# Optimization experiments

Hardware: AMD Instinct MI355X
Metric: run time of the kernel (lower is better)

## Reference

```python
import jax, jax.numpy as jnp
import numpy as np

N_NODES = 100000
N_EDGES = 3200000
N_GRAPHS = 512


def setup_inputs() -> dict:
    key = jax.random.key(0)
    ks = jax.random.split(key, 10)
    x = jax.random.normal(ks[0], (N_NODES, 2), dtype=jnp.float32)
    edge_index = jax.random.randint(ks[1], (2, N_EDGES), 0, N_NODES, dtype=jnp.int32)
    batch = jnp.sort(jax.random.randint(ks[2], (N_NODES,), 0, N_GRAPHS, dtype=jnp.int32))

    def glorot(k, shape):
        fan_in, fan_out = shape
        s = jnp.sqrt(6.0 / (fan_in + fan_out)).astype(jnp.float32)
        return jax.random.uniform(k, shape, jnp.float32, -s, s)

    return {
        "x": x,
        "edge_index": edge_index,
        "batch": batch,
        "W1": glorot(ks[3], (2, 16)),  "b1": jnp.zeros((16,), jnp.float32),
        "W2": glorot(ks[4], (16, 32)), "b2": jnp.zeros((32,), jnp.float32),
        "W3": glorot(ks[5], (32, 48)), "b3": jnp.zeros((48,), jnp.float32),
        "Wl1": glorot(ks[6], (48, 24)), "bl1": jnp.zeros((24,), jnp.float32),
        "Wl2": glorot(ks[7], (24, 10)), "bl2": jnp.zeros((10,), jnp.float32),
    }


def reference(x, edge_index, batch, W1, b1, W2, b2, W3, b3, Wl1, bl1, Wl2, bl2):
    n = x.shape[0]
    loop = jnp.arange(n, dtype=edge_index.dtype)
    # GCNConv adds self-loops, then symmetric normalization D^{-1/2} A_hat D^{-1/2}
    src = jnp.concatenate([edge_index[0], loop])  # [E+N]
    dst = jnp.concatenate([edge_index[1], loop])  # [E+N]
    deg = jax.ops.segment_sum(jnp.ones(src.shape[0], x.dtype), dst, num_segments=n)
    dis = jax.lax.rsqrt(deg)  # deg >= 1 thanks to self-loops
    norm = (dis[src] * dis[dst])[:, None]  # [E+N, 1]

    def gcn(h, W, b):
        h = h @ W  # transform first (small channel dims)
        msg = norm * h[src]  # gather + edge scale
        return jax.ops.segment_sum(msg, dst, num_segments=n) + b  # scatter-add

    h = jax.nn.relu(gcn(x, W1, b1))   # [N, 16]
    h = jax.nn.relu(gcn(h, W2, b2))   # [N, 32]
    h = jax.nn.relu(gcn(h, W3, b3))   # [N, 48]
    pooled = jax.ops.segment_max(h, batch, num_segments=N_GRAPHS)  # [G, 48]
    pooled = jnp.where(jnp.isfinite(pooled), pooled, 0.0)  # empty segments -> 0
    h = jax.nn.relu(pooled @ Wl1 + bl1)  # [G, 24]
    return h @ Wl2 + bl2  # [G, 10]
```

## Files before the change

kernel.cpp:

```cpp
#include <hip/hip_runtime.h>
#include <hip/hip_bf16.h>


#define THREADS 256
#define NBSHIFT 7
#define NPB 128
#define MAXNB 1024
#define SCAT_T 8192
#define SCAT_K 32


__global__ void bkt_count(const int* __restrict__ dst, int* __restrict__ bktCnt,
                          int nE, int nb) {
    __shared__ int h[MAXNB];
    for (int i = threadIdx.x; i < nb; i += blockDim.x) h[i] = 0;
    __syncthreads();
    for (long e = blockIdx.x * blockDim.x + threadIdx.x; e < nE;
         e += (long)gridDim.x * blockDim.x)
        atomicAdd(&h[dst[e] >> NBSHIFT], 1);
    __syncthreads();
    for (int i = threadIdx.x; i < nb; i += blockDim.x)
        if (h[i]) atomicAdd(&bktCnt[i], h[i]);
}

__global__ void bkt_scan(const int* __restrict__ bktCnt, int* __restrict__ bktBase,
                         int* __restrict__ bktCursor, int nb) {
    __shared__ int sm[MAXNB];
    int t = threadIdx.x;
    int v = (t < nb) ? bktCnt[t] : 0;
    sm[t] = v;
    __syncthreads();
    for (int o = 1; o < MAXNB; o <<= 1) {
        int add = (t >= o) ? sm[t - o] : 0;
        __syncthreads();
        sm[t] += add;
        __syncthreads();
    }
    if (t < nb) {
        int b = sm[t] - v;
        bktBase[t] = b;
        bktCursor[t] = b;
    }
}

__global__ void bkt_scatter(const int* __restrict__ src, const int* __restrict__ dst,
                            int* __restrict__ bktCursor, unsigned* __restrict__ barr,
                            int nE, int nb) {
    __shared__ int h[MAXNB];
    __shared__ int base[MAXNB];
    long t0 = (long)blockIdx.x * SCAT_T;
    for (int i = threadIdx.x; i < nb; i += blockDim.x) h[i] = 0;
    __syncthreads();
    unsigned pk[SCAT_K];
    int br[SCAT_K];
#pragma unroll
    for (int k = 0; k < SCAT_K; ++k) {
        long e = t0 + (long)k * 256 + threadIdx.x;
        if (e < nE) {
            int d = dst[e], s = src[e];
            int b = d >> NBSHIFT;
            int r = atomicAdd(&h[b], 1);
            pk[k] = (unsigned)s | ((unsigned)(d & (NPB - 1)) << 20);
            br[k] = (b << 13) | r;
        } else {
            br[k] = -1;
        }
    }
    __syncthreads();
    for (int i = threadIdx.x; i < nb; i += blockDim.x) {
        int c = h[i];
        base[i] = c ? atomicAdd(&bktCursor[i], c) : 0;
    }
    __syncthreads();
#pragma unroll
    for (int k = 0; k < SCAT_K; ++k) {
        if (br[k] >= 0) {
            int b = br[k] >> 13, r = br[k] & 8191;
            barr[(long)base[b] + r] = pk[k];
        }
    }
}

__global__ void bkt_sort(const int* __restrict__ bktBase, const int* __restrict__ bktCnt,
                         const unsigned* __restrict__ barr, int* __restrict__ col,
                         int* __restrict__ deg, int* __restrict__ rowstart, int n) {
    __shared__ int h[NPB], inc[NPB], c2[NPB];
    int b = blockIdx.x;
    int node0 = b << NBSHIFT;
    int nlocal = min(NPB, n - node0);
    int t = threadIdx.x;
    if (t < NPB) { h[t] = 0; c2[t] = 0; }
    __syncthreads();
    int base = bktBase[b], cnt = bktCnt[b];
    for (int i = t; i < cnt; i += blockDim.x)
        atomicAdd(&h[(barr[(long)base + i] >> 20) & (NPB - 1)], 1);
    __syncthreads();
    if (t < NPB) inc[t] = h[t];
    __syncthreads();
    for (int o = 1; o < NPB; o <<= 1) {
        int add = (t >= o && t < NPB) ? inc[t - o] : 0;
        __syncthreads();
        if (t < NPB) inc[t] += add;
        __syncthreads();
    }
    if (t < nlocal) {
        int node = node0 + t;
        deg[node] = h[t];
        rowstart[node] = base + inc[t] - h[t];
    }
    __syncthreads();
    for (int i = t; i < cnt; i += blockDim.x) {
        unsigned w = barr[(long)base + i];
        int dl = (w >> 20) & (NPB - 1);
        int r = atomicAdd(&c2[dl], 1);
        col[(long)base + inc[dl] - h[dl] + r] = (int)(w & 0xFFFFF);
    }
}

__global__ void dis_kernel(const int* __restrict__ deg, float* __restrict__ dis, int n) {
    int i = blockIdx.x * blockDim.x + threadIdx.x;
    if (i < n) dis[i] = 1.0f / sqrtf((float)(deg[i] + 1));
}


__global__ void pre1_kernel(const float* __restrict__ x, const float* __restrict__ dis,
                            float* __restrict__ g, int n) {
    int i = blockIdx.x * blockDim.x + threadIdx.x;
    if (i >= n) return;
    float d = dis[i];
    float2 v = ((const float2*)x)[i];
    v.x *= d; v.y *= d;
    ((float2*)g)[i] = v;
}

template <int CIN, int COUT>
__global__ void pre_kernel(const float* __restrict__ accPrev, const float* __restrict__ dis,
                           const float* __restrict__ W, const float* __restrict__ b,
                           float* __restrict__ g, int n) {
    int i = blockIdx.x * blockDim.x + threadIdx.x;
    if (i >= n) return;
    float d = dis[i];
    float a[CIN];
#pragma unroll
    for (int k = 0; k < CIN; ++k) a[k] = d * accPrev[(long)i * CIN + k];
    float o[COUT];
#pragma unroll
    for (int c = 0; c < COUT; ++c) o[c] = b[c];
#pragma unroll
    for (int k = 0; k < CIN; ++k) {
        float ak = a[k];
#pragma unroll
        for (int c = 0; c < COUT; ++c) o[c] += ak * W[k * COUT + c];
    }
#pragma unroll
    for (int c = 0; c < COUT; ++c) g[(long)i * COUT + c] = d * fmaxf(o[c], 0.0f);
}

template <int CIN, int COUT>
__global__ void final_kernel(const float* __restrict__ accPrev, const float* __restrict__ dis,
                             const float* __restrict__ W, const float* __restrict__ b,
                             float* __restrict__ h, int n) {
    int i = blockIdx.x * blockDim.x + threadIdx.x;
    if (i >= n) return;
    float d = dis[i];
    float a[CIN];
#pragma unroll
    for (int k = 0; k < CIN; ++k) a[k] = d * accPrev[(long)i * CIN + k];
    float o[COUT];
#pragma unroll
    for (int c = 0; c < COUT; ++c) o[c] = b[c];
#pragma unroll
    for (int k = 0; k < CIN; ++k) {
        float ak = a[k];
#pragma unroll
        for (int c = 0; c < COUT; ++c) o[c] += ak * W[k * COUT + c];
    }
#pragma unroll
    for (int c = 0; c < COUT; ++c) h[(long)i * COUT + c] = fmaxf(o[c], 0.0f);
}

template <int CIN>
__global__ void gather_kernel(const int* __restrict__ rowstart, const int* __restrict__ deg,
                              const int* __restrict__ col, const float* __restrict__ g,
                              float* __restrict__ acc, int n) {
    int gtid = blockIdx.x * blockDim.x + threadIdx.x;
    int node = gtid >> 6;
    int lane = threadIdx.x & 63;
    if (node >= n) return;
    constexpr int EPW = 64 / CIN;
    int c = lane % CIN;
    int es = lane / CIN;
    int base = rowstart[node];
    int dg = deg[node];
    float sum = 0.0f;
    for (int j = es; j < dg; j += EPW) {
        int s = col[base + j];
        sum += g[(long)s * CIN + c];
    }
#pragma unroll
    for (int m = CIN; m < 64; m <<= 1) sum += __shfl_xor(sum, m);
    if (lane < CIN) acc[(long)node * CIN + c] = g[(long)node * CIN + c] + sum;
}

template <int CIN>
__global__ void gather4_kernel(const int* __restrict__ rowstart, const int* __restrict__ deg,
                               const int* __restrict__ col, const float* __restrict__ g,
                               float* __restrict__ acc, int n) {
    constexpr int LPE = CIN / 4;
    constexpr int EPW = 64 / LPE;
    int gtid = blockIdx.x * blockDim.x + threadIdx.x;
    int node = gtid >> 6;
    int lane = threadIdx.x & 63;
    if (node >= n) return;
    int c4 = lane & (LPE - 1);
    int es = lane / LPE;
    int base = rowstart[node];
    int dg = deg[node];
    float4 sum = make_float4(0.f, 0.f, 0.f, 0.f);
    for (int j = es; j < dg; j += EPW) {
        int s = col[base + j];
        float4 v = ((const float4*)g)[(long)s * LPE + c4];
        sum.x += v.x; sum.y += v.y; sum.z += v.z; sum.w += v.w;
    }
#pragma unroll
    for (int m = LPE; m < 64; m <<= 1) {
        sum.x += __shfl_xor(sum.x, m);
        sum.y += __shfl_xor(sum.y, m);
        sum.z += __shfl_xor(sum.z, m);
        sum.w += __shfl_xor(sum.w, m);
    }
    if (lane < LPE) {
        float4 self = ((const float4*)g)[(long)node * LPE + c4];
        float4 r = make_float4(self.x + sum.x, self.y + sum.y,
                               self.z + sum.z, self.w + sum.w);
        ((float4*)acc)[(long)node * LPE + c4] = r;
    }
}

__global__ void pool_kernel(const float* __restrict__ h, const int* __restrict__ batch,
                            unsigned* __restrict__ pooled, int n) {
    const int C = 48, K = 16;
    int tid = blockIdx.x * blockDim.x + threadIdx.x;
    int chunk = tid / C, c = tid % C;
    int j0 = chunk * K;
    if (j0 >= n) return;
    int jend = min(j0 + K, n);
    int cur = batch[j0];
    float m = 0.0f;
    for (int j = j0; j < jend; ++j) {
        int gph = batch[j];
        if (gph != cur) {
            atomicMax(&pooled[cur * C + c], __float_as_uint(m));
            cur = gph;
            m = 0.0f;
        }
        m = fmaxf(m, h[(long)j * C + c]);
    }
    atomicMax(&pooled[cur * C + c], __float_as_uint(m));
}

__global__ void mlp_kernel(const unsigned* __restrict__ pooled, const float* __restrict__ Wl1,
                           const float* __restrict__ bl1, const float* __restrict__ Wl2,
                           const float* __restrict__ bl2, float* __restrict__ out, int G) {
    __shared__ float sW1[48 * 24];
    __shared__ float sW2[24 * 10];
    __shared__ float sp[4][48];
    __shared__ float sh[4][24];
    int t = threadIdx.x;
    int sub = t >> 6;
    int lane = t & 63;
    int g = blockIdx.x * 4 + sub;
    for (int i = t; i < 48 * 24; i += 256) sW1[i] = Wl1[i];
    for (int i = t; i < 24 * 10; i += 256) sW2[i] = Wl2[i];
    if (g < G && lane < 48) sp[sub][lane] = __uint_as_float(pooled[g * 48 + lane]);
    __syncthreads();
    if (g < G && lane < 24) {
        float a = bl1[lane];
#pragma unroll
        for (int k = 0; k < 48; ++k) a += sp[sub][k] * sW1[k * 24 + lane];
        sh[sub][lane] = fmaxf(a, 0.0f);
    }
    __syncthreads();
    if (g < G && lane < 10) {
        float a = bl2[lane];
#pragma unroll
        for (int j = 0; j < 24; ++j) a += sh[sub][j] * sW2[j * 10 + lane];
        out[g * 10 + lane] = a;
    }
}

static inline int cdiv(long a, int b) { return (int)((a + b - 1) / b); }

extern "C" void kernel_launch(void* const* d_in, const int* in_sizes, int n_in,
                              void* d_out, int out_size, void* d_ws, size_t ws_size,
                              hipStream_t stream) {
    const float* x = (const float*)d_in[0];
    const int* ei = (const int*)d_in[1];
    const int* batch = (const int*)d_in[2];
    const float* W1 = (const float*)d_in[3];
    const float* b1 = (const float*)d_in[4];
    const float* W2 = (const float*)d_in[5];
    const float* b2 = (const float*)d_in[6];
    const float* W3 = (const float*)d_in[7];
    const float* b3 = (const float*)d_in[8];
    const float* Wl1 = (const float*)d_in[9];
    const float* bl1 = (const float*)d_in[10];
    const float* Wl2 = (const float*)d_in[11];
    const float* bl2 = (const float*)d_in[12];
    float* out = (float*)d_out;

    const int N = in_sizes[0] / 2;
    const int E = in_sizes[1] / 2;
    const int G = out_size / 10;
    const int nb = cdiv(N, NPB);

    const int* src = ei;
    const int* dst = ei + E;

    char* w = (char*)d_ws;
    size_t off = 0;
    auto alloc = [&](size_t bytes) {
        void* p = w + off;
        off = (off + bytes + 255) & ~(size_t)255;
        return p;
    };
    int* bktCnt = (int*)alloc((size_t)MAXNB * 4);
    int* bktBase = (int*)alloc((size_t)MAXNB * 4);
    int* bktCursor = (int*)alloc((size_t)MAXNB * 4);
    size_t shared_bytes = ((size_t)E * 4 > (size_t)N * 48 * 4) ? (size_t)E * 4
                                                               : (size_t)N * 48 * 4;
    void* shared_region = alloc(shared_bytes);
    unsigned* barr = (unsigned*)shared_region;
    float* h3 = (float*)shared_region;
    int* col = (int*)alloc((size_t)E * 4);
    int* deg = (int*)alloc((size_t)N * 4);
    float* dis = (float*)alloc((size_t)N * 4);
    int* rowstart = (int*)alloc((size_t)N * 4);
    float* g = (float*)alloc((size_t)N * 32 * 4);
    float* acc = (float*)alloc((size_t)N * 32 * 4);
    unsigned* pooled = (unsigned*)alloc((size_t)G * 48 * 4);
    (void)ws_size;

    hipMemsetAsync(bktCnt, 0, (size_t)MAXNB * 4, stream);
    hipMemsetAsync(pooled, 0, (size_t)G * 48 * 4, stream);

    bkt_count<<<512, THREADS, 0, stream>>>(dst, bktCnt, E, nb);
    bkt_scan<<<1, MAXNB, 0, stream>>>(bktCnt, bktBase, bktCursor, nb);
    bkt_scatter<<<cdiv(E, SCAT_T), THREADS, 0, stream>>>(src, dst, bktCursor, barr, E, nb);
    bkt_sort<<<nb, THREADS, 0, stream>>>(bktBase, bktCnt, barr, col, deg, rowstart, N);
    dis_kernel<<<cdiv(N, THREADS), THREADS, 0, stream>>>(deg, dis, N);

    pre1_kernel<<<cdiv(N, THREADS), THREADS, 0, stream>>>(x, dis, g, N);
    gather_kernel<2><<<cdiv((long)N * 64, THREADS), THREADS, 0, stream>>>(
        rowstart, deg, col, g, acc, N);

    pre_kernel<2, 16><<<cdiv(N, THREADS), THREADS, 0, stream>>>(acc, dis, W1, b1, g, N);
    gather4_kernel<16><<<cdiv((long)N * 64, THREADS), THREADS, 0, stream>>>(
        rowstart, deg, col, g, acc, N);

    pre_kernel<16, 32><<<cdiv(N, THREADS), THREADS, 0, stream>>>(acc, dis, W2, b2, g, N);
    gather4_kernel<32><<<cdiv((long)N * 64, THREADS), THREADS, 0, stream>>>(
        rowstart, deg, col, g, acc, N);

    final_kernel<32, 48><<<cdiv(N, THREADS), THREADS, 0, stream>>>(acc, dis, W3, b3, h3, N);

    pool_kernel<<<cdiv((long)cdiv(N, 16) * 48, THREADS), THREADS, 0, stream>>>(h3, batch, pooled, N);

    mlp_kernel<<<cdiv(G, 4), THREADS, 0, stream>>>(pooled, Wl1, bl1, Wl2, bl2, out, G);
}
```

Measured before the change: 373.7 us.

## Store features in channel-chunked layout and gather per 8-channel chunk

The pre_kernel now writes node features in an 8-channel-chunk-major layout, and the gather becomes gather8_kernel, which processes one 32-byte chunk per launch with two nodes per wavefront. Each pass touches a smaller feature array (N*32 bytes), which is meant to raise L2 hit rates for the random neighbour gathers. The cost is that the col index array is reread once per chunk and there are more kernel launches (2 and 4 instead of 1).

```diff
diff --git a/kernel.cpp b/kernel.cpp
--- a/kernel.cpp
+++ b/kernel.cpp
@@ -153,7 +153,8 @@
         for (int c = 0; c < COUT; ++c) o[c] += ak * W[k * COUT + c];
     }
 #pragma unroll
-    for (int c = 0; c < COUT; ++c) g[(long)i * COUT + c] = d * fmaxf(o[c], 0.0f);
+    for (int c = 0; c < COUT; ++c)
+        g[((long)(c >> 3) * n + i) * 8 + (c & 7)] = d * fmaxf(o[c], 0.0f);
 }
 
 template <int CIN, int COUT>
@@ -203,37 +204,38 @@
 }
 
 template <int CIN>
-__global__ void gather4_kernel(const int* __restrict__ rowstart, const int* __restrict__ deg,
+__global__ void gather8_kernel(const int* __restrict__ rowstart, const int* __restrict__ deg,
                                const int* __restrict__ col, const float* __restrict__ g,
-                               float* __restrict__ acc, int n) {
-    constexpr int LPE = CIN / 4;
-    constexpr int EPW = 64 / LPE;
+                               float* __restrict__ acc, int n, int chunk) {
     int gtid = blockIdx.x * blockDim.x + threadIdx.x;
-    int node = gtid >> 6;
+    int wave = gtid >> 6;
     int lane = threadIdx.x & 63;
+    int node = wave * 2 + (lane >> 5);
     if (node >= n) return;
-    int c4 = lane & (LPE - 1);
-    int es = lane / LPE;
+    int l = lane & 31;
+    int c4 = l & 1;
+    int es = l >> 1;
     int base = rowstart[node];
     int dg = deg[node];
+    const float4* gc4 = (const float4*)(g + (size_t)chunk * n * 8);
     float4 sum = make_float4(0.f, 0.f, 0.f, 0.f);
-    for (int j = es; j < dg; j += EPW) {
+    for (int j = es; j < dg; j += 16) {
         int s = col[base + j];
-        float4 v = ((const float4*)g)[(long)s * LPE + c4];
+        float4 v = gc4[(long)s * 2 + c4];
         sum.x += v.x; sum.y += v.y; sum.z += v.z; sum.w += v.w;
     }
 #pragma unroll
-    for (int m = LPE; m < 64; m <<= 1) {
+    for (int m = 2; m <= 16; m <<= 1) {
         sum.x += __shfl_xor(sum.x, m);
         sum.y += __shfl_xor(sum.y, m);
         sum.z += __shfl_xor(sum.z, m);
         sum.w += __shfl_xor(sum.w, m);
     }
-    if (lane < LPE) {
-        float4 self = ((const float4*)g)[(long)node * LPE + c4];
+    if (l < 2) {
+        float4 self = gc4[(long)node * 2 + c4];
         float4 r = make_float4(self.x + sum.x, self.y + sum.y,
                                self.z + sum.z, self.w + sum.w);
-        ((float4*)acc)[(long)node * LPE + c4] = r;
+        ((float4*)acc)[(long)node * (CIN / 4) + chunk * 2 + c4] = r;
     }
 }
 
@@ -355,12 +357,14 @@
         rowstart, deg, col, g, acc, N);
 
     pre_kernel<2, 16><<<cdiv(N, THREADS), THREADS, 0, stream>>>(acc, dis, W1, b1, g, N);
-    gather4_kernel<16><<<cdiv((long)N * 64, THREADS), THREADS, 0, stream>>>(
-        rowstart, deg, col, g, acc, N);
+    for (int ch = 0; ch < 2; ++ch)
+        gather8_kernel<16><<<cdiv((long)N * 32, THREADS), THREADS, 0, stream>>>(
+            rowstart, deg, col, g, acc, N, ch);
 
     pre_kernel<16, 32><<<cdiv(N, THREADS), THREADS, 0, stream>>>(acc, dis, W2, b2, g, N);
-    gather4_kernel<32><<<cdiv((long)N * 64, THREADS), THREADS, 0, stream>>>(
-        rowstart, deg, col, g, acc, N);
+    for (int ch = 0; ch < 4; ++ch)
+        gather8_kernel<32><<<cdiv((long)N * 32, THREADS), THREADS, 0, stream>>>(
+            rowstart, deg, col, g, acc, N, ch);
 
     final_kernel<32, 48><<<cdiv(N, THREADS), THREADS, 0, stream>>>(acc, dis, W3, b3, h3, N);
 
```

Result: slower. 420.0 us (+12.4%).
